# Performance work log

Measured on AMD Instinct MI355X. Metric: run time of the kernel, lower is better.

Reference implementation:

```python
import jax, jax.numpy as jnp
import numpy as np

N_EMBD = 768
N_HEAD = 12
HEAD_DIM = N_EMBD // N_HEAD  # 64


def apply_rotary_emb(x, cos, sin):
    d = x.shape[-1] // 2
    x1, x2 = x[..., :d], x[..., d:]
    y1 = x1 * cos + x2 * sin
    y2 = x1 * -sin + x2 * cos
    return jnp.concatenate([y1, y2], axis=-1)


def rms_norm(x):
    return x * jax.lax.rsqrt(jnp.mean(jnp.square(x), axis=-1, keepdims=True) + 1e-06)


def setup_inputs() -> dict:
    key = jax.random.key(0)
    ks = jax.random.split(key, 7)
    B, T = 2, 2048
    x = jax.random.normal(ks[0], (B, T, N_EMBD), dtype=jnp.float32)
    # cos/sin broadcast over (B, head) axes of [B, T, H, HEAD_DIM//2]
    cos = jax.random.uniform(ks[1], (T, 1, HEAD_DIM // 2), dtype=jnp.float32)
    sin = jax.random.uniform(ks[2], (T, 1, HEAD_DIM // 2), dtype=jnp.float32)
    scale = 1.0 / np.sqrt(N_EMBD)
    wq = jax.random.normal(ks[3], (N_EMBD, N_EMBD), dtype=jnp.float32) * scale
    wk = jax.random.normal(ks[4], (N_EMBD, N_EMBD), dtype=jnp.float32) * scale
    wv = jax.random.normal(ks[5], (N_EMBD, N_EMBD), dtype=jnp.float32) * scale
    wproj = jax.random.normal(ks[6], (N_EMBD, N_EMBD), dtype=jnp.float32) * scale
    return {"x": x, "cos": cos, "sin": sin, "wq": wq, "wk": wk, "wv": wv, "wproj": wproj}


def reference(x, cos, sin, wq, wk, wv, wproj):
    B, T, C = x.shape
    q = (x @ wq).reshape(B, T, N_HEAD, HEAD_DIM)
    k = (x @ wk).reshape(B, T, N_HEAD, HEAD_DIM)
    v = (x @ wv).reshape(B, T, N_HEAD, HEAD_DIM)
    q = rms_norm(apply_rotary_emb(q, cos, sin))
    k = rms_norm(apply_rotary_emb(k, cos, sin))
    # [B, H, T, T] attention scores (non-causal, as in source)
    attn = jnp.einsum('bqhd,bkhd->bhqk', q, k) / jnp.sqrt(jnp.float32(HEAD_DIM))
    attn = jax.nn.softmax(attn, axis=-1)
    y = jnp.einsum('bhqk,bkhd->bqhd', attn, v).reshape(B, T, C)
    return y @ wproj
```

## Files before the change

kernel.cpp:

```cpp
#include <hip/hip_runtime.h>
#include <hip/hip_bf16.h>
#include <stdint.h>

typedef __attribute__((ext_vector_type(8))) __bf16 bf16x8;
typedef __attribute__((ext_vector_type(4))) __bf16 bf16x4;
typedef __attribute__((ext_vector_type(2))) __bf16 bf16x2;
typedef __attribute__((ext_vector_type(4))) float f32x4;
typedef __attribute__((ext_vector_type(16))) float f32x16;
typedef __attribute__((ext_vector_type(8))) unsigned short u16x8;
typedef __attribute__((ext_vector_type(4))) unsigned int u32x4;

#define DEVI __device__ __forceinline__

DEVI void gload16(const void* g, void* l) {
  __builtin_amdgcn_global_load_lds((const __attribute__((address_space(1))) void*)g,
                                   (__attribute__((address_space(3))) void*)l, 16, 0, 0);
}

DEVI uint32_t pack2(float a, float b) {
  bf16x2 t;
  t[0] = (__bf16)a;
  t[1] = (__bf16)b;
  return __builtin_bit_cast(uint32_t, t);
}

__global__ __launch_bounds__(256) void cvt_x_k(const float* __restrict__ x,
                                               __bf16* __restrict__ xb, int n4) {
  int i = blockIdx.x * blockDim.x + threadIdx.x;
  int stride = gridDim.x * blockDim.x;
  for (; i < n4; i += stride) {
    float4 v = ((const float4*)x)[i];
    bf16x4 o;
    o[0] = (__bf16)v.x; o[1] = (__bf16)v.y; o[2] = (__bf16)v.z; o[3] = (__bf16)v.w;
    ((bf16x4*)xb)[i] = o;
  }
}

__global__ __launch_bounds__(256) void wtrans_k(const float* __restrict__ wq,
                                                const float* __restrict__ wk,
                                                const float* __restrict__ wv,
                                                const float* __restrict__ wp,
                                                __bf16* __restrict__ WT) {
  __shared__ float tile[32][33];
  const float* W = (blockIdx.z == 0) ? wq : (blockIdx.z == 1) ? wk : (blockIdx.z == 2) ? wv : wp;
  int n0 = blockIdx.x * 32, k0 = blockIdx.y * 32;
  int tx = threadIdx.x, ty = threadIdx.y;
#pragma unroll
  for (int j = 0; j < 4; ++j)
    tile[ty + 8 * j][tx] = W[(size_t)(k0 + ty + 8 * j) * 768 + n0 + tx];
  __syncthreads();
#pragma unroll
  for (int j = 0; j < 4; ++j)
    WT[(size_t)(blockIdx.z * 768 + n0 + ty + 8 * j) * 768 + k0 + tx] =
        (__bf16)tile[tx][ty + 8 * j];
}

template <int EPI, int BN>
__global__ __launch_bounds__(256) void gemm_k(const __bf16* __restrict__ A,
                                              const __bf16* __restrict__ B,
                                              void* __restrict__ Cout,
                                              const float* __restrict__ cosT,
                                              const float* __restrict__ sinT,
                                              int K, int lda, int ldb, int ldc) {
  constexpr int NF = BN / 32;
  __shared__ __align__(16) __bf16 Al[128 * 32];
  __shared__ __align__(16) __bf16 Bl[BN * 32];
  const int tid = threadIdx.x, lane = tid & 63, w = tid >> 6;
  const int wm = w >> 1, wn = w & 1;
  const int m0 = blockIdx.y * 128, n0 = blockIdx.x * BN;
  const int c = lane & 15, g = lane >> 4;
  f32x4 acc[4][NF] = {};

  for (int k0 = 0; k0 < K; k0 += 32) {
#pragma unroll
    for (int i = 0; i < 2; ++i) {
      int e = (i * 256 + tid) * 8;
      int row = e >> 5, col = e & 31;
      gload16(A + (size_t)(m0 + row) * lda + k0 + col, (char*)Al + 2 * (size_t)e);
    }
#pragma unroll
    for (int i = 0; i < BN / 64; ++i) {
      int e = (i * 256 + tid) * 8;
      int row = e >> 5, col = e & 31;
      gload16(B + (size_t)(n0 + row) * ldb + k0 + col, (char*)Bl + 2 * (size_t)e);
    }
    __syncthreads();
    bf16x8 af[4], bfr[NF];
#pragma unroll
    for (int q = 0; q < 4; ++q)
      af[q] = *(const bf16x8*)&Al[(wm * 64 + q * 16 + c) * 32 + 8 * g];
#pragma unroll
    for (int q = 0; q < NF; ++q)
      bfr[q] = *(const bf16x8*)&Bl[(wn * (BN / 2) + q * 16 + c) * 32 + 8 * g];
#pragma unroll
    for (int mf = 0; mf < 4; ++mf)
#pragma unroll
      for (int nf = 0; nf < NF; ++nf)
        acc[mf][nf] = __builtin_amdgcn_mfma_f32_16x16x32_bf16(af[mf], bfr[nf],
                                                              acc[mf][nf], 0, 0, 0);
    __syncthreads();
  }

  if (EPI == 1) {
    __bf16* out = (__bf16*)Cout;
    const int colbase = n0 + wn * 64;
    const int plane = colbase / 768;
#pragma unroll
    for (int mf = 0; mf < 4; ++mf) {
#pragma unroll
      for (int r = 0; r < 4; ++r) {
        int row = m0 + wm * 64 + mf * 16 + 4 * g + r;
        float v0 = acc[mf][0][r], v1 = acc[mf][1][r], v2 = acc[mf][2][r], v3 = acc[mf][3][r];
        float y0, y1, y2, y3;
        if (plane < 2) {
          int t = row & 2047;
          float c0 = cosT[t * 32 + c],      s0 = sinT[t * 32 + c];
          float c1 = cosT[t * 32 + 16 + c], s1 = sinT[t * 32 + 16 + c];
          y0 = v0 * c0 + v2 * s0;
          y2 = v2 * c0 - v0 * s0;
          y1 = v1 * c1 + v3 * s1;
          y3 = v3 * c1 - v1 * s1;
          float ss = y0 * y0 + y1 * y1 + y2 * y2 + y3 * y3;
          ss += __shfl_xor(ss, 1); ss += __shfl_xor(ss, 2);
          ss += __shfl_xor(ss, 4); ss += __shfl_xor(ss, 8);
          float rn = rsqrtf(ss * (1.0f / 64.0f) + 1e-6f);
          y0 *= rn; y1 *= rn; y2 *= rn; y3 *= rn;
        } else {
          y0 = v0; y1 = v1; y2 = v2; y3 = v3;
        }
        size_t base = (size_t)row * ldc + colbase + c;
        out[base +  0] = (__bf16)y0;
        out[base + 16] = (__bf16)y1;
        out[base + 32] = (__bf16)y2;
        out[base + 48] = (__bf16)y3;
      }
    }
  } else {
    float* out = (float*)Cout;
#pragma unroll
    for (int mf = 0; mf < 4; ++mf)
#pragma unroll
      for (int nf = 0; nf < NF; ++nf)
#pragma unroll
        for (int r = 0; r < 4; ++r) {
          int row = m0 + wm * 64 + mf * 16 + 4 * g + r;
          out[(size_t)row * ldc + n0 + wn * (BN / 2) + nf * 16 + c] = acc[mf][nf][r];
        }
  }
}

__global__ __launch_bounds__(256, 2) void attn_k(const __bf16* __restrict__ QKV,
                                                 __bf16* __restrict__ Yb) {
  constexpr int TT = 2048;
  __shared__ __align__(16) char smem[32768];
  __bf16* Kl = (__bf16*)smem;
  const int tid = threadIdx.x, lane = tid & 63, w = tid >> 6;
  const int q5 = lane & 31, h = lane >> 5;
  const int qb = blockIdx.x, bh = blockIdx.y;
  const int b = bh / 12, hd = bh % 12;
  const size_t ldq = 2304;
  const __bf16* Qg = QKV + (size_t)(b * TT) * ldq + hd * 64;
  const __bf16* Kg = QKV + (size_t)(b * TT) * ldq + 768 + hd * 64;
  const __bf16* Vg = QKV + (size_t)(b * TT) * ldq + 1536 + hd * 64;

  const int qrow = qb * 128 + w * 32 + q5;
  bf16x8 aq[4];
#pragma unroll
  for (int t = 0; t < 4; ++t)
    aq[t] = *(const bf16x8*)(Qg + (size_t)qrow * ldq + t * 16 + 8 * h);

  f32x16 Yacc[2] = {};
  float m_run = -__builtin_inff(), l_run = 0.f;

  for (int kv0 = 0; kv0 < TT; kv0 += 128) {
#pragma unroll
    for (int p = 0; p < 4; ++p) {
      int cid = p * 256 + tid;
      int row = cid >> 3, s = cid & 7;
      int srccol = 8 * (s ^ (row & 7));
      gload16(Kg + (size_t)(kv0 + row) * ldq + srccol, (char*)Kl + row * 128 + 16 * s);
    }
#pragma unroll
    for (int p = 0; p < 2; ++p) {
      int u = p * 256 + tid;
      int kp = u >> 3, d0 = (u & 7) * 8;
      const __bf16* src0 = Vg + (size_t)(kv0 + 2 * kp) * ldq + d0;
      u16x8 v0 = *(const u16x8*)src0;
      u16x8 v1 = *(const u16x8*)(src0 + ldq);
#pragma unroll
      for (int i = 0; i < 8; ++i) {
        int d = d0 + i;
        int byte = (d * 256 + 4 * kp) ^ ((d & 15) << 4);
        uint32_t pk = (uint32_t)v0[i] | ((uint32_t)v1[i] << 16);
        *(uint32_t*)(smem + 16384 + byte) = pk;
      }
    }
    __syncthreads();

    float p_[64];
#pragma unroll
    for (int j = 0; j < 4; ++j) {
      f32x16 S = {};
#pragma unroll
      for (int t = 0; t < 4; ++t) {
        int row = j * 32 + q5;
        int chunk = (2 * t + h) ^ (q5 & 7);
        bf16x8 kf = *(const bf16x8*)((char*)Kl + row * 128 + 16 * chunk);
        S = __builtin_amdgcn_mfma_f32_32x32x16_bf16(kf, aq[t], S, 0, 0, 0);
      }
#pragma unroll
      for (int r = 0; r < 16; ++r) p_[j * 16 + r] = S[r];
    }

    float mx = p_[0];
#pragma unroll
    for (int i = 1; i < 64; ++i) mx = fmaxf(mx, p_[i]);
    mx = fmaxf(mx, __shfl_xor(mx, 32));
    float mnew = fmaxf(m_run, mx * 0.125f);
    float corr = __expf(m_run - mnew);
    float rs = 0.f;
#pragma unroll
    for (int i = 0; i < 64; ++i) {
      float p = __expf(fmaf(p_[i], 0.125f, -mnew));
      p_[i] = p;
      rs += p;
    }
    rs += __shfl_xor(rs, 32);
    l_run = l_run * corr + rs;
    m_run = mnew;
#pragma unroll
    for (int dh = 0; dh < 2; ++dh)
#pragma unroll
      for (int r = 0; r < 16; ++r) Yacc[dh][r] *= corr;

#pragma unroll
    for (int j = 0; j < 4; ++j) {
#pragma unroll
      for (int s = 0; s < 2; ++s) {
        const float* ps = p_ + j * 16 + s * 8;
        uint32_t pk01 = pack2(ps[0], ps[1]);
        uint32_t pk23 = pack2(ps[2], ps[3]);
        uint32_t pk45 = pack2(ps[4], ps[5]);
        uint32_t pk67 = pack2(ps[6], ps[7]);
        uint32_t s01 = (uint32_t)__shfl_xor((int)pk01, 32);
        uint32_t s23 = (uint32_t)__shfl_xor((int)pk23, 32);
        uint32_t s45 = (uint32_t)__shfl_xor((int)pk45, 32);
        uint32_t s67 = (uint32_t)__shfl_xor((int)pk67, 32);
        u32x4 pw;
        pw[0] = h ? s45 : pk01;
        pw[1] = h ? s67 : pk23;
        pw[2] = h ? pk45 : s01;
        pw[3] = h ? pk67 : s23;
        bf16x8 pfrag = __builtin_bit_cast(bf16x8, pw);
        int keyb = j * 64 + s * 32 + 16 * h;
#pragma unroll
        for (int dh = 0; dh < 2; ++dh) {
          int d = dh * 32 + q5;
          int byte = (d * 256 + keyb) ^ ((d & 15) << 4);
          bf16x8 vf = *(const bf16x8*)(smem + 16384 + byte);
          Yacc[dh] = __builtin_amdgcn_mfma_f32_32x32x16_bf16(vf, pfrag, Yacc[dh], 0, 0, 0);
        }
      }
    }
    __syncthreads();
  }

  float rl = __builtin_amdgcn_rcpf(l_run);
  char* yb = smem + w * (32 * 144);
#pragma unroll
  for (int dh = 0; dh < 2; ++dh)
#pragma unroll
    for (int a = 0; a < 4; ++a) {
      bf16x4 pkv;
#pragma unroll
      for (int i = 0; i < 4; ++i) pkv[i] = (__bf16)(Yacc[dh][a * 4 + i] * rl);
      int d0 = a * 8 + 4 * h + 32 * dh;
      *(bf16x4*)(yb + q5 * 144 + d0 * 2) = pkv;
    }
  __bf16* Yrow = Yb + (size_t)(b * TT + qb * 128 + w * 32) * 768 + hd * 64;
#pragma unroll
  for (int k = 0; k < 4; ++k) {
    int chunk = k * 64 + lane;
    int qr = chunk >> 3, sr = chunk & 7;
    bf16x8 vv = *(const bf16x8*)(yb + qr * 144 + sr * 16);
    *(bf16x8*)(Yrow + (size_t)qr * 768 + sr * 8) = vv;
  }
}

extern "C" void kernel_launch(void* const* d_in, const int* in_sizes, int n_in,
                              void* d_out, int out_size, void* d_ws, size_t ws_size,
                              hipStream_t stream) {
  const float* x = (const float*)d_in[0];
  const float* cosT = (const float*)d_in[1];
  const float* sinT = (const float*)d_in[2];
  const float* wq = (const float*)d_in[3];
  const float* wk = (const float*)d_in[4];
  const float* wv = (const float*)d_in[5];
  const float* wp = (const float*)d_in[6];

  char* ws = (char*)d_ws;
  __bf16* xb   = (__bf16*)(ws);
  __bf16* WT   = (__bf16*)(ws + 6291456);
  __bf16* QKVb = (__bf16*)(ws + 11010048);
  __bf16* Yb   = (__bf16*)(ws + 29884416);

  cvt_x_k<<<2048, 256, 0, stream>>>(x, xb, (4096 * 768) / 4);
  wtrans_k<<<dim3(24, 24, 4), dim3(32, 8), 0, stream>>>(wq, wk, wv, wp, WT);
  gemm_k<1, 128><<<dim3(18, 32), 256, 0, stream>>>(xb, WT, (void*)QKVb, cosT, sinT,
                                                   768, 768, 768, 2304);
  attn_k<<<dim3(16, 24), 256, 0, stream>>>(QKVb, Yb);
  gemm_k<0, 64><<<dim3(12, 32), 256, 0, stream>>>(Yb, WT + (size_t)2304 * 768, d_out,
                                                  nullptr, nullptr, 768, 768, 768, 768);
}
```

Before: 202.5 us.

## Double-buffer GEMM and attention tiles, add lazy softmax rescale and cheaper shuffles

```diff
diff --git a/kernel.cpp b/kernel.cpp
--- a/kernel.cpp
+++ b/kernel.cpp
@@ -23,6 +23,8 @@
   t[1] = (__bf16)b;
   return __builtin_bit_cast(uint32_t, t);
 }
+
+DEVI int vswz(int d) { return ((d ^ (d >> 3)) & 15) << 4; }
 
 __global__ __launch_bounds__(256) void cvt_x_k(const float* __restrict__ x,
                                                __bf16* __restrict__ xb, int n4) {
@@ -63,35 +65,42 @@
                                               const float* __restrict__ sinT,
                                               int K, int lda, int ldb, int ldc) {
   constexpr int NF = BN / 32;
-  __shared__ __align__(16) __bf16 Al[128 * 32];
-  __shared__ __align__(16) __bf16 Bl[BN * 32];
+  __shared__ __align__(16) __bf16 Al[2][128 * 32];
+  __shared__ __align__(16) __bf16 Bl[2][BN * 32];
   const int tid = threadIdx.x, lane = tid & 63, w = tid >> 6;
   const int wm = w >> 1, wn = w & 1;
   const int m0 = blockIdx.y * 128, n0 = blockIdx.x * BN;
   const int c = lane & 15, g = lane >> 4;
   f32x4 acc[4][NF] = {};
 
-  for (int k0 = 0; k0 < K; k0 += 32) {
+  auto stage = [&](int k0, int buf) {
 #pragma unroll
     for (int i = 0; i < 2; ++i) {
       int e = (i * 256 + tid) * 8;
       int row = e >> 5, col = e & 31;
-      gload16(A + (size_t)(m0 + row) * lda + k0 + col, (char*)Al + 2 * (size_t)e);
+      gload16(A + (size_t)(m0 + row) * lda + k0 + col, (char*)&Al[buf][0] + 2 * (size_t)e);
     }
 #pragma unroll
     for (int i = 0; i < BN / 64; ++i) {
       int e = (i * 256 + tid) * 8;
       int row = e >> 5, col = e & 31;
-      gload16(B + (size_t)(n0 + row) * ldb + k0 + col, (char*)Bl + 2 * (size_t)e);
-    }
-    __syncthreads();
+      gload16(B + (size_t)(n0 + row) * ldb + k0 + col, (char*)&Bl[buf][0] + 2 * (size_t)e);
+    }
+  };
+
+  stage(0, 0);
+  __syncthreads();
+  const int NIT = K / 32;
+  for (int t = 0; t < NIT; ++t) {
+    const int cur = t & 1;
+    if (t + 1 < NIT) stage((t + 1) * 32, cur ^ 1);
     bf16x8 af[4], bfr[NF];
 #pragma unroll
     for (int q = 0; q < 4; ++q)
-      af[q] = *(const bf16x8*)&Al[(wm * 64 + q * 16 + c) * 32 + 8 * g];
+      af[q] = *(const bf16x8*)&Al[cur][(wm * 64 + q * 16 + c) * 32 + 8 * g];
 #pragma unroll
     for (int q = 0; q < NF; ++q)
-      bfr[q] = *(const bf16x8*)&Bl[(wn * (BN / 2) + q * 16 + c) * 32 + 8 * g];
+      bfr[q] = *(const bf16x8*)&Bl[cur][(wn * (BN / 2) + q * 16 + c) * 32 + 8 * g];
 #pragma unroll
     for (int mf = 0; mf < 4; ++mf)
 #pragma unroll
@@ -152,8 +161,8 @@
 __global__ __launch_bounds__(256, 2) void attn_k(const __bf16* __restrict__ QKV,
                                                  __bf16* __restrict__ Yb) {
   constexpr int TT = 2048;
-  __shared__ __align__(16) char smem[32768];
-  __bf16* Kl = (__bf16*)smem;
+  constexpr int NT = TT / 128;
+  __shared__ __align__(16) char smem[65536];
   const int tid = threadIdx.x, lane = tid & 63, w = tid >> 6;
   const int q5 = lane & 31, h = lane >> 5;
   const int qb = blockIdx.x, bh = blockIdx.y;
@@ -169,69 +178,107 @@
   for (int t = 0; t < 4; ++t)
     aq[t] = *(const bf16x8*)(Qg + (size_t)qrow * ldq + t * 16 + 8 * h);
 
-  f32x16 Yacc[2] = {};
-  float m_run = -__builtin_inff(), l_run = 0.f;
-
-  for (int kv0 = 0; kv0 < TT; kv0 += 128) {
+  u16x8 vr[4];
+  auto stageK = [&](int kv0, int buf) {
 #pragma unroll
     for (int p = 0; p < 4; ++p) {
       int cid = p * 256 + tid;
       int row = cid >> 3, s = cid & 7;
       int srccol = 8 * (s ^ (row & 7));
-      gload16(Kg + (size_t)(kv0 + row) * ldq + srccol, (char*)Kl + row * 128 + 16 * s);
-    }
+      gload16(Kg + (size_t)(kv0 + row) * ldq + srccol,
+              smem + buf * 16384 + row * 128 + 16 * s);
+    }
+  };
+  auto loadV = [&](int kv0) {
 #pragma unroll
     for (int p = 0; p < 2; ++p) {
       int u = p * 256 + tid;
       int kp = u >> 3, d0 = (u & 7) * 8;
       const __bf16* src0 = Vg + (size_t)(kv0 + 2 * kp) * ldq + d0;
-      u16x8 v0 = *(const u16x8*)src0;
-      u16x8 v1 = *(const u16x8*)(src0 + ldq);
+      vr[2 * p] = *(const u16x8*)src0;
+      vr[2 * p + 1] = *(const u16x8*)(src0 + ldq);
+    }
+  };
+  auto writeV = [&](int buf) {
+    char* vb = smem + 32768 + buf * 16384;
+#pragma unroll
+    for (int p = 0; p < 2; ++p) {
+      int u = p * 256 + tid;
+      int kp = u >> 3, d0 = (u & 7) * 8;
 #pragma unroll
       for (int i = 0; i < 8; ++i) {
         int d = d0 + i;
-        int byte = (d * 256 + 4 * kp) ^ ((d & 15) << 4);
-        uint32_t pk = (uint32_t)v0[i] | ((uint32_t)v1[i] << 16);
-        *(uint32_t*)(smem + 16384 + byte) = pk;
+        int byte = (d * 256 + 4 * kp) ^ vswz(d);
+        uint32_t pk = (uint32_t)vr[2 * p][i] | ((uint32_t)vr[2 * p + 1][i] << 16);
+        *(uint32_t*)(vb + byte) = pk;
       }
     }
-    __syncthreads();
+  };
+
+  f32x16 Yacc[2] = {};
+  float m_run = -__builtin_inff(), l_run = 0.f;
+
+  stageK(0, 0);
+  loadV(0);
+  writeV(0);
+  __syncthreads();
+
+  for (int t = 0; t < NT; ++t) {
+    const int cur = t & 1;
+    const char* Kb = smem + cur * 16384;
+    const char* Vb = smem + 32768 + cur * 16384;
+    if (t + 1 < NT) {
+      stageK((t + 1) * 128, cur ^ 1);
+      loadV((t + 1) * 128);
+    }
 
     float p_[64];
 #pragma unroll
     for (int j = 0; j < 4; ++j) {
       f32x16 S = {};
 #pragma unroll
-      for (int t = 0; t < 4; ++t) {
+      for (int tt = 0; tt < 4; ++tt) {
         int row = j * 32 + q5;
-        int chunk = (2 * t + h) ^ (q5 & 7);
-        bf16x8 kf = *(const bf16x8*)((char*)Kl + row * 128 + 16 * chunk);
-        S = __builtin_amdgcn_mfma_f32_32x32x16_bf16(kf, aq[t], S, 0, 0, 0);
+        int chunk = (2 * tt + h) ^ (q5 & 7);
+        bf16x8 kf = *(const bf16x8*)(Kb + row * 128 + 16 * chunk);
+        S = __builtin_amdgcn_mfma_f32_32x32x16_bf16(kf, aq[tt], S, 0, 0, 0);
       }
 #pragma unroll
       for (int r = 0; r < 16; ++r) p_[j * 16 + r] = S[r];
     }
 
-    float mx = p_[0];
-#pragma unroll
-    for (int i = 1; i < 64; ++i) mx = fmaxf(mx, p_[i]);
+    float m0 = p_[0], m1 = p_[1], m2 = p_[2], m3 = p_[3];
+#pragma unroll
+    for (int i = 4; i < 64; i += 4) {
+      m0 = fmaxf(m0, p_[i]);     m1 = fmaxf(m1, p_[i + 1]);
+      m2 = fmaxf(m2, p_[i + 2]); m3 = fmaxf(m3, p_[i + 3]);
+    }
+    float mx = fmaxf(fmaxf(m0, m1), fmaxf(m2, m3));
     mx = fmaxf(mx, __shfl_xor(mx, 32));
-    float mnew = fmaxf(m_run, mx * 0.125f);
-    float corr = __expf(m_run - mnew);
-    float rs = 0.f;
-#pragma unroll
-    for (int i = 0; i < 64; ++i) {
-      float p = __expf(fmaf(p_[i], 0.125f, -mnew));
-      p_[i] = p;
-      rs += p;
-    }
+    mx *= 0.125f;
+    if (!__all(mx <= m_run + 5.545f)) {
+      float mnew = fmaxf(m_run, mx);
+      float corr = __expf(m_run - mnew);
+      l_run *= corr;
+#pragma unroll
+      for (int dh = 0; dh < 2; ++dh)
+#pragma unroll
+        for (int r = 0; r < 16; ++r) Yacc[dh][r] *= corr;
+      m_run = mnew;
+    }
+    float rs0 = 0.f, rs1 = 0.f, rs2 = 0.f, rs3 = 0.f;
+#pragma unroll
+    for (int i = 0; i < 64; i += 4) {
+      float e0 = __expf(fmaf(p_[i], 0.125f, -m_run));
+      float e1 = __expf(fmaf(p_[i + 1], 0.125f, -m_run));
+      float e2 = __expf(fmaf(p_[i + 2], 0.125f, -m_run));
+      float e3 = __expf(fmaf(p_[i + 3], 0.125f, -m_run));
+      p_[i] = e0; p_[i + 1] = e1; p_[i + 2] = e2; p_[i + 3] = e3;
+      rs0 += e0; rs1 += e1; rs2 += e2; rs3 += e3;
+    }
+    float rs = (rs0 + rs1) + (rs2 + rs3);
     rs += __shfl_xor(rs, 32);
-    l_run = l_run * corr + rs;
-    m_run = mnew;
-#pragma unroll
-    for (int dh = 0; dh < 2; ++dh)
-#pragma unroll
-      for (int r = 0; r < 16; ++r) Yacc[dh][r] *= corr;
+    l_run += rs;
 
 #pragma unroll
     for (int j = 0; j < 4; ++j) {
@@ -242,26 +289,25 @@
         uint32_t pk23 = pack2(ps[2], ps[3]);
         uint32_t pk45 = pack2(ps[4], ps[5]);
         uint32_t pk67 = pack2(ps[6], ps[7]);
-        uint32_t s01 = (uint32_t)__shfl_xor((int)pk01, 32);
-        uint32_t s23 = (uint32_t)__shfl_xor((int)pk23, 32);
-        uint32_t s45 = (uint32_t)__shfl_xor((int)pk45, 32);
-        uint32_t s67 = (uint32_t)__shfl_xor((int)pk67, 32);
+        uint32_t fa = (uint32_t)__shfl_xor((int)(h ? pk01 : pk45), 32);
+        uint32_t fb = (uint32_t)__shfl_xor((int)(h ? pk23 : pk67), 32);
         u32x4 pw;
-        pw[0] = h ? s45 : pk01;
-        pw[1] = h ? s67 : pk23;
-        pw[2] = h ? pk45 : s01;
-        pw[3] = h ? pk67 : s23;
+        pw[0] = h ? fa : pk01;
+        pw[1] = h ? fb : pk23;
+        pw[2] = h ? pk45 : fa;
+        pw[3] = h ? pk67 : fb;
         bf16x8 pfrag = __builtin_bit_cast(bf16x8, pw);
         int keyb = j * 64 + s * 32 + 16 * h;
 #pragma unroll
         for (int dh = 0; dh < 2; ++dh) {
           int d = dh * 32 + q5;
-          int byte = (d * 256 + keyb) ^ ((d & 15) << 4);
-          bf16x8 vf = *(const bf16x8*)(smem + 16384 + byte);
+          int byte = (d * 256 + keyb) ^ vswz(d);
+          bf16x8 vf = *(const bf16x8*)(Vb + byte);
           Yacc[dh] = __builtin_amdgcn_mfma_f32_32x32x16_bf16(vf, pfrag, Yacc[dh], 0, 0, 0);
         }
       }
     }
+    if (t + 1 < NT) writeV(cur ^ 1);
     __syncthreads();
   }
 
```

New measurement: 181.6 us. -10.3%, faster.
